# Performance work log

Hardware: AMD Instinct MI355X
Metric: run time of the kernel (lower is better)

## Reference

```python
import jax, jax.numpy as jnp
import numpy as np

B, C, N = 16, 7, 32768  # batch, keypoints per animal, frames


def setup_inputs() -> dict:
    key = jax.random.key(0)
    k1, k2 = jax.random.split(key)
    # pixel-scale coordinates, (B, 2C, N, 2)
    x = jax.random.normal(k1, (B, 2 * C, N, 2), dtype=jnp.float32) * 100.0
    # context: [..., circle_flag, arena_w, arena_h]
    context = jax.random.uniform(k2, (B, 3), dtype=jnp.float32)
    return {"x": x, "context": context}


def _norm(a):
    return jnp.linalg.norm(a, axis=-1)


def _dot(a, b):
    return jnp.sum(a * b, axis=-1)


def _features(x, context):
    _, C2, _, _ = x.shape
    Cq = C2 // 2
    x1, x2 = x[:, :Cq], x[:, Cq:]  # (B, C, N, 2) each

    # per-animal displacements (first step is zero via prepend)
    dx1 = jnp.diff(x1, axis=2, prepend=x1[:, :, :1])
    dx2 = jnp.diff(x2, axis=2, prepend=x2[:, :, :1])
    n1, n2 = _norm(dx1), _norm(dx2)

    # turning cosine between consecutive displacement vectors, zero-prepended
    adx1 = _dot(dx1[:, :, 1:], dx1[:, :, :-1]) / (n1[:, :, 1:] * n1[:, :, :-1] + 1e-4)
    adx1 = jnp.concatenate([jnp.zeros_like(adx1[:, :, :1]), adx1], axis=2)
    adx2 = _dot(dx2[:, :, 1:], dx2[:, :, :-1]) / (n2[:, :, 1:] * n2[:, :, :-1] + 1e-4)
    adx2 = jnp.concatenate([jnp.zeros_like(adx2[:, :, :1]), adx2], axis=2)

    # acceleration and 2D cross product (signed curvature-like term)
    ddx1 = jnp.diff(dx1, axis=2, prepend=dx1[:, :, :1])
    ddx2 = jnp.diff(dx2, axis=2, prepend=dx2[:, :, :1])
    cross1 = dx1[..., 0] * ddx1[..., 1] - dx1[..., 1] * ddx1[..., 0]
    cross2 = dx2[..., 0] * ddx2[..., 1] - dx2[..., 1] * ddx2[..., 0]

    # direction alignment between the two animals
    dirs = _dot(dx1, dx2) / (n1 * n2 + 1e-6)

    # relative position / leading cosines
    rel_x = x1 - x2
    nrel = _norm(rel_x)
    lead1 = _dot(dx1, rel_x) / (n1 * nrel + 1e-6)
    lead2 = _dot(dx2, -rel_x) / (n2 * nrel + 1e-6)

    # all-pairs keypoint distances via channel rolls: torch roll(s): out[j] = in[(j - s) % C]
    roll_idx = (jnp.arange(Cq)[None, :] - jnp.arange(1, Cq + 1)[:, None]) % Cq  # (C, C)
    x1r = x1[:, roll_idx.reshape(-1)]  # (B, C*C, N, 2), rolls stacked along channels
    x2t = jnp.tile(x2, (1, Cq, 1, 1))
    d = _norm(x1r - x2t + 1e-6)  # PairwiseDistance eps=1e-6 added inside the norm

    # forward diff of d with a trailing zero appended
    dd = jnp.diff(jnp.concatenate([d, jnp.zeros_like(d[:, :, :1])], axis=2), axis=-1)

    # (B, 9*C + 2*C*C, N)
    return jnp.concatenate(
        [n1, n2, cross1, cross2, adx1, adx2, dirs, d, dd, lead1, lead2], axis=1
    )


def reference(x, context):
    return _features(x, context)
```

## Files before the change

### kernel.cpp

```cpp
#include <hip/hip_runtime.h>

#define CC 7
#define NN 32768
#define NCH 161
#define SPAN 256
#define W    264

typedef float vfloat4 __attribute__((ext_vector_type(4)));

__device__ __forceinline__ void stnt4(float* p, float4 v) {
    vfloat4 w = {v.x, v.y, v.z, v.w};
    __builtin_nontemporal_store(w, (vfloat4*)p);
}
__device__ __forceinline__ float frcp(float x) { return __builtin_amdgcn_rcpf(x); }
__device__ __forceinline__ float fsq(float x)  { return __builtin_amdgcn_sqrtf(x); }

__global__ __launch_bounds__(256) void feat_kernel(const float* __restrict__ x,
                                                   float* __restrict__ out) {
    __shared__ float S[2 * CC][2][W];
    const int t  = threadIdx.x;
    const int N0 = blockIdx.x * SPAN;
    const int b  = blockIdx.y;

    const float* xb = x + (size_t)b * (2 * CC) * NN * 2;

    for (int idx = t; idx < 2 * CC * (W / 2); idx += 256) {
        int ch = idx / (W / 2);
        int m  = idx - ch * (W / 2);
        int g0 = N0 - 2 + 2 * m;
        const float* p = xb + (size_t)ch * NN * 2;
        float4 v;
        if (g0 >= 0 && g0 + 1 < NN) {
            v = *(const float4*)(p + 2 * g0);
        } else {
            int ga = g0     < 0 ? 0 : (g0     > NN - 1 ? NN - 1 : g0);
            int gb = g0 + 1 < 0 ? 0 : (g0 + 1 > NN - 1 ? NN - 1 : g0 + 1);
            float2 va = *(const float2*)(p + 2 * ga);
            float2 vb = *(const float2*)(p + 2 * gb);
            v = make_float4(va.x, va.y, vb.x, vb.y);
        }
        *(float2*)&S[ch][0][2 * m] = make_float2(v.x, v.z);
        *(float2*)&S[ch][1][2 * m] = make_float2(v.y, v.w);
    }
    __syncthreads();

    const int wg = t >> 6;
    const int tl = t & 63;
    const int p0 = 4 * tl;
    float* ob = out + (size_t)b * NCH * NN + N0 + 4 * tl;

#pragma unroll
    for (int it = 0; it < 4; ++it) {
        const int ch = it * 4 + wg;
        if (ch < 14) {
            float4 X0 = *(const float4*)&S[ch][0][p0];
            float4 X1 = *(const float4*)&S[ch][0][p0 + 4];
            float4 Y0 = *(const float4*)&S[ch][1][p0];
            float4 Y1 = *(const float4*)&S[ch][1][p0 + 4];
            float wx[6] = {X0.x, X0.y, X0.z, X0.w, X1.x, X1.y};
            float wy[6] = {Y0.x, Y0.y, Y0.z, Y0.w, Y1.x, Y1.y};
            float dx[5], dy[5], nr[5];
#pragma unroll
            for (int m = 0; m < 5; ++m) {
                dx[m] = wx[m + 1] - wx[m];
                dy[m] = wy[m + 1] - wy[m];
                nr[m] = fsq(dx[m] * dx[m] + dy[m] * dy[m]);
            }
            float4 on, oc, oa;
            float* vn = &on.x; float* vc = &oc.x; float* va = &oa.x;
#pragma unroll
            for (int k = 0; k < 4; ++k) {
                vn[k] = nr[k + 1];
                vc[k] = dx[k + 1] * (dy[k + 1] - dy[k]) - dy[k + 1] * (dx[k + 1] - dx[k]);
                va[k] = (dx[k + 1] * dx[k] + dy[k + 1] * dy[k]) * frcp(nr[k + 1] * nr[k] + 1e-4f);
            }
            stnt4(ob + (size_t)(ch) * NN,      on);
            stnt4(ob + (size_t)(14 + ch) * NN, oc);
            stnt4(ob + (size_t)(28 + ch) * NN, oa);
        }
    }

#pragma unroll
    for (int it = 0; it < 2; ++it) {
        const int c = it * 4 + wg;
        if (c < 7) {
            float4 AX0 = *(const float4*)&S[c][0][p0];
            float4 AX1 = *(const float4*)&S[c][0][p0 + 4];
            float4 AY0 = *(const float4*)&S[c][1][p0];
            float4 AY1 = *(const float4*)&S[c][1][p0 + 4];
            float4 BX0 = *(const float4*)&S[c + CC][0][p0];
            float4 BX1 = *(const float4*)&S[c + CC][0][p0 + 4];
            float4 BY0 = *(const float4*)&S[c + CC][1][p0];
            float4 BY1 = *(const float4*)&S[c + CC][1][p0 + 4];
            float w1x[5] = {AX0.y, AX0.z, AX0.w, AX1.x, AX1.y};
            float w1y[5] = {AY0.y, AY0.z, AY0.w, AY1.x, AY1.y};
            float w2x[5] = {BX0.y, BX0.z, BX0.w, BX1.x, BX1.y};
            float w2y[5] = {BY0.y, BY0.z, BY0.w, BY1.x, BY1.y};
            float4 od, ol1, ol2;
            float* vd = &od.x; float* v1 = &ol1.x; float* v2 = &ol2.x;
#pragma unroll
            for (int k = 0; k < 4; ++k) {
                float d1x = w1x[k + 1] - w1x[k], d1y = w1y[k + 1] - w1y[k];
                float d2x = w2x[k + 1] - w2x[k], d2y = w2y[k + 1] - w2y[k];
                float n1 = fsq(d1x * d1x + d1y * d1y);
                float n2 = fsq(d2x * d2x + d2y * d2y);
                float rx = w1x[k + 1] - w2x[k + 1], ry = w1y[k + 1] - w2y[k + 1];
                float nr = fsq(rx * rx + ry * ry);
                vd[k] = (d1x * d2x + d1y * d2y) * frcp(n1 * n2 + 1e-6f);
                v1[k] = (d1x * rx + d1y * ry) * frcp(n1 * nr + 1e-6f);
                v2[k] = -(d2x * rx + d2y * ry) * frcp(n2 * nr + 1e-6f);
            }
            stnt4(ob + (size_t)(42 + c) * NN,  od);
            stnt4(ob + (size_t)(147 + c) * NN, ol1);
            stnt4(ob + (size_t)(154 + c) * NN, ol2);
        }
    }

    const bool lastpt = (N0 + 4 * tl + 4 == NN);
    for (int j = wg; j < 7; j += 4) {
        float4 BX0 = *(const float4*)&S[CC + j][0][p0];
        float4 BX1 = *(const float4*)&S[CC + j][0][p0 + 4];
        float4 BY0 = *(const float4*)&S[CC + j][1][p0];
        float4 BY1 = *(const float4*)&S[CC + j][1][p0 + 4];
        float w2x[5] = {BX0.z, BX0.w, BX1.x, BX1.y, BX1.z};
        float w2y[5] = {BY0.z, BY0.w, BY1.x, BY1.y, BY1.z};
#pragma unroll
        for (int i = 0; i < 7; ++i) {
            int c1 = j - i - 1;
            c1 = (c1 < 0) ? c1 + 7 : c1;
            float4 AX0 = *(const float4*)&S[c1][0][p0];
            float4 AX1 = *(const float4*)&S[c1][0][p0 + 4];
            float4 AY0 = *(const float4*)&S[c1][1][p0];
            float4 AY1 = *(const float4*)&S[c1][1][p0 + 4];
            float w1x[5] = {AX0.z, AX0.w, AX1.x, AX1.y, AX1.z};
            float w1y[5] = {AY0.z, AY0.w, AY1.x, AY1.y, AY1.z};
            float d[5];
#pragma unroll
            for (int p = 0; p < 5; ++p) {
                float ddx = w1x[p] - w2x[p] + 1e-6f;
                float ddy = w1y[p] - w2y[p] + 1e-6f;
                d[p] = fsq(ddx * ddx + ddy * ddy);
            }
            float dd3 = lastpt ? -d[3] : d[4] - d[3];
            const int pair = i * 7 + j;
            stnt4(ob + (size_t)(49 + pair) * NN,
                  make_float4(d[0], d[1], d[2], d[3]));
            stnt4(ob + (size_t)(98 + pair) * NN,
                  make_float4(d[1] - d[0], d[2] - d[1], d[3] - d[2], dd3));
        }
    }
}

extern "C" void kernel_launch(void* const* d_in, const int* in_sizes, int n_in,
                              void* d_out, int out_size, void* d_ws, size_t ws_size,
                              hipStream_t stream) {
    const float* x = (const float*)d_in[0];
    float* out = (float*)d_out;
    dim3 grid(NN / SPAN, 16);
    feat_kernel<<<grid, 256, 0, stream>>>(x, out);
}
```

Baseline: 68.07 us.

## Double block span to 512 frames and rebalance pairwise work across eight waves

Each block now covers 512 frames with 512 threads, and each wave handles two 256-frame halves. The 49 pairwise-distance channels are split into near-equal compile-time ranges over eight waves instead of a strided per-j loop over four waves, and the direction/lead phase is given to waves 1-7 so wave 0 takes an extra pairwise share. The aim is to even out per-wave load, cut halo overhead and reduce the number of blocks. In exchange there are fewer blocks (1024), higher register and LDS use per block, and the per-pair loop reloads the B channel from LDS for every pair.

Result: slower. 74.75 us (+9.8%).

```diff
diff --git a/kernel.cpp b/kernel.cpp
--- a/kernel.cpp
+++ b/kernel.cpp
@@ -3,8 +3,8 @@
 #define CC 7
 #define NN 32768
 #define NCH 161
-#define SPAN 256
-#define W    264
+#define SPAN 512
+#define W    520
 
 typedef float vfloat4 __attribute__((ext_vector_type(4)));
 
@@ -15,7 +15,52 @@
 __device__ __forceinline__ float frcp(float x) { return __builtin_amdgcn_rcpf(x); }
 __device__ __forceinline__ float fsq(float x)  { return __builtin_amdgcn_sqrtf(x); }
 
-__global__ __launch_bounds__(256) void feat_kernel(const float* __restrict__ x,
+template <int LO, int HI>
+__device__ __forceinline__ void phase3(const float (*S)[2][W], float* ob,
+                                       int tl, int N0) {
+#pragma unroll
+    for (int pp = LO; pp < HI; ++pp) {
+        const int j = pp / 7;
+        const int i = pp % 7;
+        int c1 = j - i - 1;
+        c1 = (c1 < 0) ? c1 + 7 : c1;
+        const int pair = i * 7 + j;
+        float4 od[2], odd[2];
+#pragma unroll
+        for (int h = 0; h < 2; ++h) {
+            const int p0 = 4 * tl + 256 * h;
+            float4 BX0 = *(const float4*)&S[CC + j][0][p0];
+            float4 BX1 = *(const float4*)&S[CC + j][0][p0 + 4];
+            float4 BY0 = *(const float4*)&S[CC + j][1][p0];
+            float4 BY1 = *(const float4*)&S[CC + j][1][p0 + 4];
+            float4 AX0 = *(const float4*)&S[c1][0][p0];
+            float4 AX1 = *(const float4*)&S[c1][0][p0 + 4];
+            float4 AY0 = *(const float4*)&S[c1][1][p0];
+            float4 AY1 = *(const float4*)&S[c1][1][p0 + 4];
+            float w1x[5] = {AX0.z, AX0.w, AX1.x, AX1.y, AX1.z};
+            float w1y[5] = {AY0.z, AY0.w, AY1.x, AY1.y, AY1.z};
+            float w2x[5] = {BX0.z, BX0.w, BX1.x, BX1.y, BX1.z};
+            float w2y[5] = {BY0.z, BY0.w, BY1.x, BY1.y, BY1.z};
+            float d[5];
+#pragma unroll
+            for (int p = 0; p < 5; ++p) {
+                float ddx = w1x[p] - w2x[p] + 1e-6f;
+                float ddy = w1y[p] - w2y[p] + 1e-6f;
+                d[p] = fsq(ddx * ddx + ddy * ddy);
+            }
+            const bool lastpt = (N0 + 256 * h + 4 * tl + 4 == NN);
+            float dd3 = lastpt ? -d[3] : d[4] - d[3];
+            od[h]  = make_float4(d[0], d[1], d[2], d[3]);
+            odd[h] = make_float4(d[1] - d[0], d[2] - d[1], d[3] - d[2], dd3);
+        }
+        stnt4(ob + (size_t)(49 + pair) * NN,       od[0]);
+        stnt4(ob + (size_t)(49 + pair) * NN + 256, od[1]);
+        stnt4(ob + (size_t)(98 + pair) * NN,       odd[0]);
+        stnt4(ob + (size_t)(98 + pair) * NN + 256, odd[1]);
+    }
+}
+
+__global__ __launch_bounds__(512) void feat_kernel(const float* __restrict__ x,
                                                    float* __restrict__ out) {
     __shared__ float S[2 * CC][2][W];
     const int t  = threadIdx.x;
@@ -24,7 +69,7 @@
 
     const float* xb = x + (size_t)b * (2 * CC) * NN * 2;
 
-    for (int idx = t; idx < 2 * CC * (W / 2); idx += 256) {
+    for (int idx = t; idx < 2 * CC * (W / 2); idx += 512) {
         int ch = idx / (W / 2);
         int m  = idx - ch * (W / 2);
         int g0 = N0 - 2 + 2 * m;
@@ -46,44 +91,52 @@
 
     const int wg = t >> 6;
     const int tl = t & 63;
-    const int p0 = 4 * tl;
     float* ob = out + (size_t)b * NCH * NN + N0 + 4 * tl;
 
 #pragma unroll
-    for (int it = 0; it < 4; ++it) {
-        const int ch = it * 4 + wg;
+    for (int it = 0; it < 2; ++it) {
+        const int ch = wg + 8 * it;
         if (ch < 14) {
-            float4 X0 = *(const float4*)&S[ch][0][p0];
-            float4 X1 = *(const float4*)&S[ch][0][p0 + 4];
-            float4 Y0 = *(const float4*)&S[ch][1][p0];
-            float4 Y1 = *(const float4*)&S[ch][1][p0 + 4];
-            float wx[6] = {X0.x, X0.y, X0.z, X0.w, X1.x, X1.y};
-            float wy[6] = {Y0.x, Y0.y, Y0.z, Y0.w, Y1.x, Y1.y};
-            float dx[5], dy[5], nr[5];
+            float4 on[2], oc[2], oa[2];
 #pragma unroll
-            for (int m = 0; m < 5; ++m) {
-                dx[m] = wx[m + 1] - wx[m];
-                dy[m] = wy[m + 1] - wy[m];
-                nr[m] = fsq(dx[m] * dx[m] + dy[m] * dy[m]);
+            for (int h = 0; h < 2; ++h) {
+                const int p0 = 4 * tl + 256 * h;
+                float4 X0 = *(const float4*)&S[ch][0][p0];
+                float4 X1 = *(const float4*)&S[ch][0][p0 + 4];
+                float4 Y0 = *(const float4*)&S[ch][1][p0];
+                float4 Y1 = *(const float4*)&S[ch][1][p0 + 4];
+                float wx[6] = {X0.x, X0.y, X0.z, X0.w, X1.x, X1.y};
+                float wy[6] = {Y0.x, Y0.y, Y0.z, Y0.w, Y1.x, Y1.y};
+                float dx[5], dy[5], nr[5];
+#pragma unroll
+                for (int m = 0; m < 5; ++m) {
+                    dx[m] = wx[m + 1] - wx[m];
+                    dy[m] = wy[m + 1] - wy[m];
+                    nr[m] = fsq(dx[m] * dx[m] + dy[m] * dy[m]);
+                }
+                float* vn = &on[h].x; float* vc = &oc[h].x; float* va = &oa[h].x;
+#pragma unroll
+                for (int k = 0; k < 4; ++k) {
+                    vn[k] = nr[k + 1];
+                    vc[k] = dx[k + 1] * (dy[k + 1] - dy[k]) - dy[k + 1] * (dx[k + 1] - dx[k]);
+                    va[k] = (dx[k + 1] * dx[k] + dy[k + 1] * dy[k]) * frcp(nr[k + 1] * nr[k] + 1e-4f);
+                }
             }
-            float4 on, oc, oa;
-            float* vn = &on.x; float* vc = &oc.x; float* va = &oa.x;
-#pragma unroll
-            for (int k = 0; k < 4; ++k) {
-                vn[k] = nr[k + 1];
-                vc[k] = dx[k + 1] * (dy[k + 1] - dy[k]) - dy[k + 1] * (dx[k + 1] - dx[k]);
-                va[k] = (dx[k + 1] * dx[k] + dy[k + 1] * dy[k]) * frcp(nr[k + 1] * nr[k] + 1e-4f);
-            }
-            stnt4(ob + (size_t)(ch) * NN,      on);
-            stnt4(ob + (size_t)(14 + ch) * NN, oc);
-            stnt4(ob + (size_t)(28 + ch) * NN, oa);
+            stnt4(ob + (size_t)(ch) * NN,            on[0]);
+            stnt4(ob + (size_t)(ch) * NN + 256,      on[1]);
+            stnt4(ob + (size_t)(14 + ch) * NN,       oc[0]);
+            stnt4(ob + (size_t)(14 + ch) * NN + 256, oc[1]);
+            stnt4(ob + (size_t)(28 + ch) * NN,       oa[0]);
+            stnt4(ob + (size_t)(28 + ch) * NN + 256, oa[1]);
         }
     }
 
+    if (wg > 0) {
+        const int c = wg - 1;
+        float4 od[2], ol1[2], ol2[2];
 #pragma unroll
-    for (int it = 0; it < 2; ++it) {
-        const int c = it * 4 + wg;
-        if (c < 7) {
+        for (int h = 0; h < 2; ++h) {
+            const int p0 = 4 * tl + 256 * h;
             float4 AX0 = *(const float4*)&S[c][0][p0];
             float4 AX1 = *(const float4*)&S[c][0][p0 + 4];
             float4 AY0 = *(const float4*)&S[c][1][p0];
@@ -96,8 +149,7 @@
             float w1y[5] = {AY0.y, AY0.z, AY0.w, AY1.x, AY1.y};
             float w2x[5] = {BX0.y, BX0.z, BX0.w, BX1.x, BX1.y};
             float w2y[5] = {BY0.y, BY0.z, BY0.w, BY1.x, BY1.y};
-            float4 od, ol1, ol2;
-            float* vd = &od.x; float* v1 = &ol1.x; float* v2 = &ol2.x;
+            float* vd = &od[h].x; float* v1 = &ol1[h].x; float* v2 = &ol2[h].x;
 #pragma unroll
             for (int k = 0; k < 4; ++k) {
                 float d1x = w1x[k + 1] - w1x[k], d1y = w1y[k + 1] - w1y[k];
@@ -110,44 +162,24 @@
                 v1[k] = (d1x * rx + d1y * ry) * frcp(n1 * nr + 1e-6f);
                 v2[k] = -(d2x * rx + d2y * ry) * frcp(n2 * nr + 1e-6f);
             }
-            stnt4(ob + (size_t)(42 + c) * NN,  od);
-            stnt4(ob + (size_t)(147 + c) * NN, ol1);
-            stnt4(ob + (size_t)(154 + c) * NN, ol2);
         }
+        stnt4(ob + (size_t)(42 + c) * NN,        od[0]);
+        stnt4(ob + (size_t)(42 + c) * NN + 256,  od[1]);
+        stnt4(ob + (size_t)(147 + c) * NN,       ol1[0]);
+        stnt4(ob + (size_t)(147 + c) * NN + 256, ol1[1]);
+        stnt4(ob + (size_t)(154 + c) * NN,       ol2[0]);
+        stnt4(ob + (size_t)(154 + c) * NN + 256, ol2[1]);
     }
 
-    const bool lastpt = (N0 + 4 * tl + 4 == NN);
-    for (int j = wg; j < 7; j += 4) {
-        float4 BX0 = *(const float4*)&S[CC + j][0][p0];
-        float4 BX1 = *(const float4*)&S[CC + j][0][p0 + 4];
-        float4 BY0 = *(const float4*)&S[CC + j][1][p0];
-        float4 BY1 = *(const float4*)&S[CC + j][1][p0 + 4];
-        float w2x[5] = {BX0.z, BX0.w, BX1.x, BX1.y, BX1.z};
-        float w2y[5] = {BY0.z, BY0.w, BY1.x, BY1.y, BY1.z};
-#pragma unroll
-        for (int i = 0; i < 7; ++i) {
-            int c1 = j - i - 1;
-            c1 = (c1 < 0) ? c1 + 7 : c1;
-            float4 AX0 = *(const float4*)&S[c1][0][p0];
-            float4 AX1 = *(const float4*)&S[c1][0][p0 + 4];
-            float4 AY0 = *(const float4*)&S[c1][1][p0];
-            float4 AY1 = *(const float4*)&S[c1][1][p0 + 4];
-            float w1x[5] = {AX0.z, AX0.w, AX1.x, AX1.y, AX1.z};
-            float w1y[5] = {AY0.z, AY0.w, AY1.x, AY1.y, AY1.z};
-            float d[5];
-#pragma unroll
-            for (int p = 0; p < 5; ++p) {
-                float ddx = w1x[p] - w2x[p] + 1e-6f;
-                float ddy = w1y[p] - w2y[p] + 1e-6f;
-                d[p] = fsq(ddx * ddx + ddy * ddy);
-            }
-            float dd3 = lastpt ? -d[3] : d[4] - d[3];
-            const int pair = i * 7 + j;
-            stnt4(ob + (size_t)(49 + pair) * NN,
-                  make_float4(d[0], d[1], d[2], d[3]));
-            stnt4(ob + (size_t)(98 + pair) * NN,
-                  make_float4(d[1] - d[0], d[2] - d[1], d[3] - d[2], dd3));
-        }
+    switch (wg) {
+        case 0: phase3<0, 7>(S, ob, tl, N0); break;
+        case 1: phase3<7, 13>(S, ob, tl, N0); break;
+        case 2: phase3<13, 19>(S, ob, tl, N0); break;
+        case 3: phase3<19, 25>(S, ob, tl, N0); break;
+        case 4: phase3<25, 31>(S, ob, tl, N0); break;
+        case 5: phase3<31, 37>(S, ob, tl, N0); break;
+        case 6: phase3<37, 43>(S, ob, tl, N0); break;
+        default: phase3<43, 49>(S, ob, tl, N0); break;
     }
 }
 
@@ -157,5 +189,5 @@
     const float* x = (const float*)d_in[0];
     float* out = (float*)d_out;
     dim3 grid(NN / SPAN, 16);
-    feat_kernel<<<grid, 256, 0, stream>>>(x, out);
+    feat_kernel<<<grid, 512, 0, stream>>>(x, out);
 }
```
